# Optimization experiments

Hardware: AMD Instinct MI355X
Metric: run time of the kernel (lower is better)

Reference implementation:

```python
import jax, jax.numpy as jnp
import numpy as np

GAMMA = 2.0  # focal focusing parameter
LAM = 0.1    # disco weight


def _centered_dist(x, nw):
    """Doubly (weighted) centered pairwise |x_i - x_j| matrix, as in distance_corr."""
    d = jnp.abs(x[:, None] - x[None, :])          # [N, N]
    davg = jnp.mean(d * nw, axis=1)               # [N]  (row-wise weighted mean)
    return d - davg[None, :] - davg[:, None] + jnp.mean(davg * nw)


def _dcorr(Amat, Bmat, nw):
    ABavg = jnp.mean(Amat * Bmat * nw, axis=1)
    AAavg = jnp.mean(Amat * Amat * nw, axis=1)
    BBavg = jnp.mean(Bmat * Bmat * nw, axis=1)
    return jnp.mean(ABavg * nw) / jnp.sqrt(jnp.mean(AAavg * nw) * jnp.mean(BBavg * nw))


def setup_inputs() -> dict:
    key = jax.random.key(0)
    k1, k2, k3, k4 = jax.random.split(key, 4)
    N, C = 8192, 4
    return {
        "outputs": jax.random.normal(k1, (N, C), dtype=jnp.float32),
        "labels": jax.random.randint(k2, (N,), 0, C, dtype=jnp.int32),
        "event": jax.random.normal(k3, (N,), dtype=jnp.float32),
        "weights": jax.random.uniform(k4, (N, 1), dtype=jnp.float32, minval=0.1, maxval=1.0),
    }


def reference(outputs, labels, event, weights):
    N, C = outputs.shape
    w = weights.squeeze()                          # [N]

    # Focal loss (reduction='none'), alpha=None
    logp = jax.nn.log_softmax(outputs, axis=1)     # [N, C]
    logpt = logp[jnp.arange(N), labels]            # [N]
    pt = jnp.exp(logpt)
    focal = -(1.0 - pt) ** GAMMA * logpt * w       # per-example, times weights

    probs = jnp.exp(logp)                          # softmax(outputs)
    nw = w * N / jnp.sum(w)                        # normed weights (sum == N)

    # event-side centered distance matrix is class-independent: compute once
    Bmat = _centered_dist(event, nw)               # [N, N]

    disco = jnp.float32(0.0)
    for i in range(C):                             # small fixed class loop
        Amat = _centered_dist(probs[:, i], nw)
        disco = disco + _dcorr(Amat, Bmat, nw)
    disco = disco / C

    f = jnp.mean(focal)
    return jnp.stack([f, disco, f + LAM * disco])  # [focal, disco, tot]
```

## Files before the change

kernel.cpp:

```cpp
#include <hip/hip_runtime.h>
#include <math.h>

#define BLK 256
#define IT 2
#define JSPLIT 32
#define LAM 0.1f


__device__ __forceinline__ float wave_reduce(float v) {
    v += __shfl_down(v, 32, 64);
    v += __shfl_down(v, 16, 64);
    v += __shfl_down(v, 8, 64);
    v += __shfl_down(v, 4, 64);
    v += __shfl_down(v, 2, 64);
    v += __shfl_down(v, 1, 64);
    return v;
}

__global__ __launch_bounds__(BLK) void k1_rowprep(
        const float* __restrict__ outs, const int* __restrict__ labels,
        const float* __restrict__ event, const float* __restrict__ wts,
        float* __restrict__ probs, float* __restrict__ rows,
        float* __restrict__ scal, float* __restrict__ kpart, int N) {
    __shared__ float red[4][12];
    int i = blockIdx.x * BLK + threadIdx.x;
    float4 o = ((const float4*)outs)[i];
    float m = fmaxf(fmaxf(o.x, o.y), fmaxf(o.z, o.w));
    float e0 = expf(o.x - m), e1 = expf(o.y - m), e2 = expf(o.z - m), e3 = expf(o.w - m);
    float s = e0 + e1 + e2 + e3;
    float inv = 1.0f / s;
    float4 p = make_float4(e0 * inv, e1 * inv, e2 * inv, e3 * inv);
    ((float4*)probs)[i] = p;

    int l = labels[i];
    float ol = (l == 0) ? o.x : (l == 1) ? o.y : (l == 2) ? o.z : o.w;
    float logpt = ol - m - logf(s);
    float pt = expf(logpt);
    float w = wts[i];
    float ev = event[i];
    float om = 1.0f - pt;
    float focal = -om * om * logpt * w;

#pragma unroll
    for (int v = 0; v < 5; ++v) rows[v * N + i] = 0.f;
    if (blockIdx.x == 0 && threadIdx.x < 4) scal[threadIdx.x] = 0.f;

    float vals[12] = {focal, w,
                      w * p.x, w * p.y, w * p.z, w * p.w, w * ev,
                      w * p.x * p.x, w * p.y * p.y, w * p.z * p.z,
                      w * p.w * p.w, w * ev * ev};
    int lane = threadIdx.x & 63, wave = threadIdx.x >> 6;
#pragma unroll
    for (int k = 0; k < 12; ++k) {
        float r = wave_reduce(vals[k]);
        if (lane == 0) red[wave][k] = r;
    }
    __syncthreads();
    if (threadIdx.x < 12)
        kpart[blockIdx.x * 12 + threadIdx.x] =
            red[0][threadIdx.x] + red[1][threadIdx.x] + red[2][threadIdx.x] + red[3][threadIdx.x];
}

__global__ __launch_bounds__(BLK) void k2_pairs(
        const float* __restrict__ probs, const float* __restrict__ event,
        const float* __restrict__ wts, float* __restrict__ rows,
        float* __restrict__ scal, int N) {
    __shared__ float4 jp[BLK];
    __shared__ float2 jew[BLK];
    __shared__ float red[4][4];

    int tid = threadIdx.x;
    int i0 = blockIdx.x * (BLK * IT) + tid;
    int i1 = i0 + BLK;
    float4 pA = ((const float4*)probs)[i0];
    float4 pB = ((const float4*)probs)[i1];
    float eA = event[i0], eB = event[i1];
    float wA = wts[i0], wB = wts[i1];

    int jcount = N / JSPLIT;
    int jbase = blockIdx.y * jcount;

    float sA0 = 0.f, sA1 = 0.f, sA2 = 0.f, sA3 = 0.f, sAe = 0.f;
    float sB0 = 0.f, sB1 = 0.f, sB2 = 0.f, sB3 = 0.f, sBe = 0.f;
    float tA0 = 0.f, tA1 = 0.f, tA2 = 0.f, tA3 = 0.f;
    float tB0 = 0.f, tB1 = 0.f, tB2 = 0.f, tB3 = 0.f;

    for (int jc = 0; jc < jcount; jc += BLK) {
        int j = jbase + jc + tid;
        jp[tid] = ((const float4*)probs)[j];
        jew[tid] = make_float2(event[j], wts[j]);
        __syncthreads();
#pragma unroll 4
        for (int jj = 0; jj < BLK; ++jj) {
            float4 p = jp[jj];
            float2 ew = jew[jj];
            float wj = ew.y;
            {
                float d0 = fabsf(pA.x - p.x);
                float d1 = fabsf(pA.y - p.y);
                float d2 = fabsf(pA.z - p.z);
                float d3 = fabsf(pA.w - p.w);
                float de = fabsf(eA - ew.x);
                sA0 = fmaf(wj, d0, sA0);
                sA1 = fmaf(wj, d1, sA1);
                sA2 = fmaf(wj, d2, sA2);
                sA3 = fmaf(wj, d3, sA3);
                sAe = fmaf(wj, de, sAe);
                float wde = wj * de;
                tA0 = fmaf(wde, d0, tA0);
                tA1 = fmaf(wde, d1, tA1);
                tA2 = fmaf(wde, d2, tA2);
                tA3 = fmaf(wde, d3, tA3);
            }
            {
                float d0 = fabsf(pB.x - p.x);
                float d1 = fabsf(pB.y - p.y);
                float d2 = fabsf(pB.z - p.z);
                float d3 = fabsf(pB.w - p.w);
                float de = fabsf(eB - ew.x);
                sB0 = fmaf(wj, d0, sB0);
                sB1 = fmaf(wj, d1, sB1);
                sB2 = fmaf(wj, d2, sB2);
                sB3 = fmaf(wj, d3, sB3);
                sBe = fmaf(wj, de, sBe);
                float wde = wj * de;
                tB0 = fmaf(wde, d0, tB0);
                tB1 = fmaf(wde, d1, tB1);
                tB2 = fmaf(wde, d2, tB2);
                tB3 = fmaf(wde, d3, tB3);
            }
        }
        __syncthreads();
    }

    atomicAdd(&rows[0 * N + i0], sA0);
    atomicAdd(&rows[1 * N + i0], sA1);
    atomicAdd(&rows[2 * N + i0], sA2);
    atomicAdd(&rows[3 * N + i0], sA3);
    atomicAdd(&rows[4 * N + i0], sAe);
    atomicAdd(&rows[0 * N + i1], sB0);
    atomicAdd(&rows[1 * N + i1], sB1);
    atomicAdd(&rows[2 * N + i1], sB2);
    atomicAdd(&rows[3 * N + i1], sB3);
    atomicAdd(&rows[4 * N + i1], sBe);

    float t0 = tA0 * wA + tB0 * wB;
    float t1 = tA1 * wA + tB1 * wB;
    float t2 = tA2 * wA + tB2 * wB;
    float t3 = tA3 * wA + tB3 * wB;
    int lane = tid & 63, wave = tid >> 6;
    t0 = wave_reduce(t0); t1 = wave_reduce(t1);
    t2 = wave_reduce(t2); t3 = wave_reduce(t3);
    if (lane == 0) {
        red[wave][0] = t0; red[wave][1] = t1;
        red[wave][2] = t2; red[wave][3] = t3;
    }
    __syncthreads();
    if (tid < 4)
        atomicAdd(&scal[tid], red[0][tid] + red[1][tid] + red[2][tid] + red[3][tid]);
}

__global__ __launch_bounds__(1024) void k3_final(
        const float* __restrict__ rows, const float* __restrict__ scal,
        const float* __restrict__ wts, const float* __restrict__ kpart,
        float* __restrict__ out, int N) {
    __shared__ float red[16][14];
    __shared__ float fin[12];
    int tid = threadIdx.x, lane = tid & 63, wave = tid >> 6;

    if (wave == 0) {
#pragma unroll
        for (int k = 0; k < 12; ++k) {
            float v = (lane < 32) ? kpart[lane * 12 + k] : 0.f;
            v = wave_reduce(v);
            if (lane == 0) fin[k] = v;
        }
    }

    float acc[14];
#pragma unroll
    for (int k = 0; k < 14; ++k) acc[k] = 0.f;

    for (int i = tid; i < N; i += 1024) {
        float w = wts[i];
        float s0 = rows[0 * N + i], s1 = rows[1 * N + i], s2 = rows[2 * N + i],
              s3 = rows[3 * N + i], sE = rows[4 * N + i];
        acc[0] += w * s0; acc[1] += w * s1; acc[2] += w * s2;
        acc[3] += w * s3; acc[4] += w * sE;
        float wE = w * sE;
        acc[5] += wE * s0; acc[6] += wE * s1; acc[7] += wE * s2; acc[8] += wE * s3;
        acc[9] += wE * sE;
        acc[10] += w * s0 * s0; acc[11] += w * s1 * s1;
        acc[12] += w * s2 * s2; acc[13] += w * s3 * s3;
    }

#pragma unroll
    for (int k = 0; k < 14; ++k) acc[k] = wave_reduce(acc[k]);
    if (lane == 0) {
#pragma unroll
        for (int k = 0; k < 14; ++k) red[wave][k] = acc[k];
    }
    __syncthreads();

    if (tid == 0) {
        float SW[5], SWW_ce[4], SWW_ee, SWW_cc[4];
#pragma unroll
        for (int k = 0; k < 5; ++k) {
            float a = 0.f;
            for (int wv = 0; wv < 16; ++wv) a += red[wv][k];
            SW[k] = a;
        }
#pragma unroll
        for (int k = 0; k < 4; ++k) {
            float a = 0.f;
            for (int wv = 0; wv < 16; ++wv) a += red[wv][5 + k];
            SWW_ce[k] = a;
        }
        {
            float a = 0.f;
            for (int wv = 0; wv < 16; ++wv) a += red[wv][9];
            SWW_ee = a;
        }
#pragma unroll
        for (int k = 0; k < 4; ++k) {
            float a = 0.f;
            for (int wv = 0; wv < 16; ++wv) a += red[wv][10 + k];
            SWW_cc[k] = a;
        }

        float focal_sum = fin[0];
        float W = fin[1];
        float M1[5] = {fin[2], fin[3], fin[4], fin[5], fin[6]};
        float M2[5] = {fin[7], fin[8], fin[9], fin[10], fin[11]};

        float invW2 = 1.0f / (W * W);
        float invW3 = invW2 / W;

        float g[5];
#pragma unroll
        for (int v = 0; v < 5; ++v) g[v] = SW[v] * invW2;
        float gE = g[4];

        float Tee = 2.0f * (W * M2[4] - M1[4] * M1[4]);
        float num_ee = Tee * invW2 - 2.0f * SWW_ee * invW3 + gE * gE;

        float disco = 0.f;
#pragma unroll
        for (int c = 0; c < 4; ++c) {
            float Tcc = 2.0f * (W * M2[c] - M1[c] * M1[c]);
            float num_cc = Tcc * invW2 - 2.0f * SWW_cc[c] * invW3 + g[c] * g[c];
            float num_ce = scal[c] * invW2 - 2.0f * SWW_ce[c] * invW3 + g[c] * gE;
            disco += num_ce * rsqrtf(num_cc * num_ee);
        }
        disco *= 0.25f;

        float f = focal_sum / (float)N;
        out[0] = f;
        out[1] = disco;
        out[2] = f + LAM * disco;
    }
}

extern "C" void kernel_launch(void* const* d_in, const int* in_sizes, int n_in,
                              void* d_out, int out_size, void* d_ws, size_t ws_size,
                              hipStream_t stream) {
    const float* outs = (const float*)d_in[0];
    const int* labels = (const int*)d_in[1];
    const float* event = (const float*)d_in[2];
    const float* wts = (const float*)d_in[3];
    float* out = (float*)d_out;
    int N = in_sizes[1];

    float* ws = (float*)d_ws;
    float* probs = ws;
    float* rows = probs + (size_t)N * 4;
    float* scal = rows + (size_t)N * 5;
    float* kpart = scal + 16;

    k1_rowprep<<<N / BLK, BLK, 0, stream>>>(outs, labels, event, wts, probs, rows, scal, kpart, N);

    dim3 g2(N / (BLK * IT), JSPLIT);
    k2_pairs<<<g2, BLK, 0, stream>>>(probs, event, wts, rows, scal, N);

    k3_final<<<1, 1024, 0, stream>>>(rows, scal, wts, kpart, out, N);
}
```

Baseline: 113.2 us.

## Fuse three kernels into one cooperative kernel with grid syncs

Replaces the three separate launches (row prep, pairwise sums, final reduction) with one cooperative kernel of 1024 blocks that uses grid.sync between phases. The j dimension is split 64 ways, so each block handles a single 128-element tile with no tile loop. The aim is to cut launch overhead and inter-kernel gaps, and to run more blocks so the pairwise phase fills more of the GPU. Costs are two grid-wide barriers, a final reduction done by a single 256-thread block, and a fallback to the old three-kernel path if the cooperative launch fails (for example, if 1024 resident blocks do not fit).

```diff
diff --git a/kernel.cpp b/kernel.cpp
--- a/kernel.cpp
+++ b/kernel.cpp
@@ -1,9 +1,13 @@
 #include <hip/hip_runtime.h>
+#include <hip/hip_cooperative_groups.h>
 #include <math.h>
+
+namespace cg = cooperative_groups;
 
 #define BLK 256
 #define IT 2
-#define JSPLIT 32
+#define JSPLIT 64
+#define NBLOCKS 1024
 #define LAM 0.1f
 
 
@@ -17,81 +21,92 @@
     return v;
 }
 
-__global__ __launch_bounds__(BLK) void k1_rowprep(
+__global__ __launch_bounds__(BLK, 4) void fused_all(
         const float* __restrict__ outs, const int* __restrict__ labels,
         const float* __restrict__ event, const float* __restrict__ wts,
         float* __restrict__ probs, float* __restrict__ rows,
-        float* __restrict__ scal, float* __restrict__ kpart, int N) {
-    __shared__ float red[4][12];
-    int i = blockIdx.x * BLK + threadIdx.x;
-    float4 o = ((const float4*)outs)[i];
-    float m = fmaxf(fmaxf(o.x, o.y), fmaxf(o.z, o.w));
-    float e0 = expf(o.x - m), e1 = expf(o.y - m), e2 = expf(o.z - m), e3 = expf(o.w - m);
-    float s = e0 + e1 + e2 + e3;
-    float inv = 1.0f / s;
-    float4 p = make_float4(e0 * inv, e1 * inv, e2 * inv, e3 * inv);
-    ((float4*)probs)[i] = p;
-
-    int l = labels[i];
-    float ol = (l == 0) ? o.x : (l == 1) ? o.y : (l == 2) ? o.z : o.w;
-    float logpt = ol - m - logf(s);
-    float pt = expf(logpt);
-    float w = wts[i];
-    float ev = event[i];
-    float om = 1.0f - pt;
-    float focal = -om * om * logpt * w;
-
-#pragma unroll
-    for (int v = 0; v < 5; ++v) rows[v * N + i] = 0.f;
-    if (blockIdx.x == 0 && threadIdx.x < 4) scal[threadIdx.x] = 0.f;
-
-    float vals[12] = {focal, w,
-                      w * p.x, w * p.y, w * p.z, w * p.w, w * ev,
-                      w * p.x * p.x, w * p.y * p.y, w * p.z * p.z,
-                      w * p.w * p.w, w * ev * ev};
-    int lane = threadIdx.x & 63, wave = threadIdx.x >> 6;
-#pragma unroll
-    for (int k = 0; k < 12; ++k) {
-        float r = wave_reduce(vals[k]);
-        if (lane == 0) red[wave][k] = r;
-    }
-    __syncthreads();
-    if (threadIdx.x < 12)
-        kpart[blockIdx.x * 12 + threadIdx.x] =
-            red[0][threadIdx.x] + red[1][threadIdx.x] + red[2][threadIdx.x] + red[3][threadIdx.x];
-}
-
-__global__ __launch_bounds__(BLK) void k2_pairs(
-        const float* __restrict__ probs, const float* __restrict__ event,
-        const float* __restrict__ wts, float* __restrict__ rows,
-        float* __restrict__ scal, int N) {
-    __shared__ float4 jp[BLK];
-    __shared__ float2 jew[BLK];
-    __shared__ float red[4][4];
+        float* __restrict__ scal, float* __restrict__ kpart,
+        float* __restrict__ out, int N) {
+    cg::grid_group grid = cg::this_grid();
+
+    __shared__ float4 jp[128];
+    __shared__ float2 jew[128];
+    __shared__ float red[16][14];
+    __shared__ float fin[12];
 
     int tid = threadIdx.x;
-    int i0 = blockIdx.x * (BLK * IT) + tid;
-    int i1 = i0 + BLK;
-    float4 pA = ((const float4*)probs)[i0];
-    float4 pB = ((const float4*)probs)[i1];
-    float eA = event[i0], eB = event[i1];
-    float wA = wts[i0], wB = wts[i1];
-
-    int jcount = N / JSPLIT;
-    int jbase = blockIdx.y * jcount;
-
-    float sA0 = 0.f, sA1 = 0.f, sA2 = 0.f, sA3 = 0.f, sAe = 0.f;
-    float sB0 = 0.f, sB1 = 0.f, sB2 = 0.f, sB3 = 0.f, sBe = 0.f;
-    float tA0 = 0.f, tA1 = 0.f, tA2 = 0.f, tA3 = 0.f;
-    float tB0 = 0.f, tB1 = 0.f, tB2 = 0.f, tB3 = 0.f;
-
-    for (int jc = 0; jc < jcount; jc += BLK) {
-        int j = jbase + jc + tid;
-        jp[tid] = ((const float4*)probs)[j];
-        jew[tid] = make_float2(event[j], wts[j]);
+    int b = blockIdx.x;
+    int lane = tid & 63, wave = tid >> 6;
+
+    {
+        int gid = b * BLK + tid;
+        if (gid < 5 * N + 16) rows[gid] = 0.f;
+
+        if (b < N / BLK) {
+            int i = b * BLK + tid;
+            float4 o = ((const float4*)outs)[i];
+            float m = fmaxf(fmaxf(o.x, o.y), fmaxf(o.z, o.w));
+            float e0 = expf(o.x - m), e1 = expf(o.y - m),
+                  e2 = expf(o.z - m), e3 = expf(o.w - m);
+            float s = e0 + e1 + e2 + e3;
+            float inv = 1.0f / s;
+            float4 p = make_float4(e0 * inv, e1 * inv, e2 * inv, e3 * inv);
+            ((float4*)probs)[i] = p;
+
+            int l = labels[i];
+            float ol = (l == 0) ? o.x : (l == 1) ? o.y : (l == 2) ? o.z : o.w;
+            float logpt = ol - m - logf(s);
+            float pt = expf(logpt);
+            float w = wts[i];
+            float ev = event[i];
+            float om = 1.0f - pt;
+            float focal = -om * om * logpt * w;
+
+            float vals[12] = {focal, w,
+                              w * p.x, w * p.y, w * p.z, w * p.w, w * ev,
+                              w * p.x * p.x, w * p.y * p.y, w * p.z * p.z,
+                              w * p.w * p.w, w * ev * ev};
+#pragma unroll
+            for (int k = 0; k < 12; ++k) {
+                float r = wave_reduce(vals[k]);
+                if (lane == 0) red[wave][k] = r;
+            }
+            __syncthreads();
+            if (tid < 12)
+                kpart[b * 12 + tid] =
+                    red[0][tid] + red[1][tid] + red[2][tid] + red[3][tid];
+        }
+    }
+
+    grid.sync();
+
+    {
+        int itile = b & 15;
+        int jsp = b >> 4;
+        int jcount = N / JSPLIT;
+        int jbase = jsp * jcount;
+
+        int i0 = itile * (BLK * IT) + tid;
+        int i1 = i0 + BLK;
+        float4 pA = ((const float4*)probs)[i0];
+        float4 pB = ((const float4*)probs)[i1];
+        float eA = event[i0], eB = event[i1];
+        float wA = wts[i0], wB = wts[i1];
+
+        if (tid < 128) {
+            int j = jbase + tid;
+            jp[tid] = ((const float4*)probs)[j];
+            jew[tid] = make_float2(event[j], wts[j]);
+        }
         __syncthreads();
+
+        float sA0 = 0.f, sA1 = 0.f, sA2 = 0.f, sA3 = 0.f, sAe = 0.f;
+        float sB0 = 0.f, sB1 = 0.f, sB2 = 0.f, sB3 = 0.f, sBe = 0.f;
+        float tA0 = 0.f, tA1 = 0.f, tA2 = 0.f, tA3 = 0.f;
+        float tB0 = 0.f, tB1 = 0.f, tB2 = 0.f, tB3 = 0.f;
+
 #pragma unroll 4
-        for (int jj = 0; jj < BLK; ++jj) {
+        for (int jj = 0; jj < 128; ++jj) {
             float4 p = jp[jj];
             float2 ew = jew[jj];
             float wj = ew.y;
@@ -130,24 +145,223 @@
                 tB3 = fmaf(wde, d3, tB3);
             }
         }
+
+        atomicAdd(&rows[0 * N + i0], sA0);
+        atomicAdd(&rows[1 * N + i0], sA1);
+        atomicAdd(&rows[2 * N + i0], sA2);
+        atomicAdd(&rows[3 * N + i0], sA3);
+        atomicAdd(&rows[4 * N + i0], sAe);
+        atomicAdd(&rows[0 * N + i1], sB0);
+        atomicAdd(&rows[1 * N + i1], sB1);
+        atomicAdd(&rows[2 * N + i1], sB2);
+        atomicAdd(&rows[3 * N + i1], sB3);
+        atomicAdd(&rows[4 * N + i1], sBe);
+
+        float t0 = tA0 * wA + tB0 * wB;
+        float t1 = tA1 * wA + tB1 * wB;
+        float t2 = tA2 * wA + tB2 * wB;
+        float t3 = tA3 * wA + tB3 * wB;
+        t0 = wave_reduce(t0); t1 = wave_reduce(t1);
+        t2 = wave_reduce(t2); t3 = wave_reduce(t3);
         __syncthreads();
-    }
-
-    atomicAdd(&rows[0 * N + i0], sA0);
-    atomicAdd(&rows[1 * N + i0], sA1);
-    atomicAdd(&rows[2 * N + i0], sA2);
-    atomicAdd(&rows[3 * N + i0], sA3);
+        if (lane == 0) {
+            red[wave][0] = t0; red[wave][1] = t1;
+            red[wave][2] = t2; red[wave][3] = t3;
+        }
+        __syncthreads();
+        if (tid < 4)
+            atomicAdd(&scal[tid],
+                      red[0][tid] + red[1][tid] + red[2][tid] + red[3][tid]);
+    }
+
+    grid.sync();
+
+    if (b == 0) {
+        if (wave == 0) {
+#pragma unroll
+            for (int k = 0; k < 12; ++k) {
+                float v = (lane < 32) ? kpart[lane * 12 + k] : 0.f;
+                v = wave_reduce(v);
+                if (lane == 0) fin[k] = v;
+            }
+        }
+
+        float acc[14];
+#pragma unroll
+        for (int k = 0; k < 14; ++k) acc[k] = 0.f;
+
+        for (int i = tid; i < N; i += BLK) {
+            float w = wts[i];
+            float s0 = rows[0 * N + i], s1 = rows[1 * N + i],
+                  s2 = rows[2 * N + i], s3 = rows[3 * N + i],
+                  sE = rows[4 * N + i];
+            acc[0] += w * s0; acc[1] += w * s1; acc[2] += w * s2;
+            acc[3] += w * s3; acc[4] += w * sE;
+            float wE = w * sE;
+            acc[5] += wE * s0; acc[6] += wE * s1;
+            acc[7] += wE * s2; acc[8] += wE * s3;
+            acc[9] += wE * sE;
+            acc[10] += w * s0 * s0; acc[11] += w * s1 * s1;
+            acc[12] += w * s2 * s2; acc[13] += w * s3 * s3;
+        }
+
+#pragma unroll
+        for (int k = 0; k < 14; ++k) acc[k] = wave_reduce(acc[k]);
+        __syncthreads();
+        if (lane == 0) {
+#pragma unroll
+            for (int k = 0; k < 14; ++k) red[wave][k] = acc[k];
+        }
+        __syncthreads();
+
+        if (tid == 0) {
+            float SW[5], SWW_ce[4], SWW_ee, SWW_cc[4];
+#pragma unroll
+            for (int k = 0; k < 5; ++k)
+                SW[k] = red[0][k] + red[1][k] + red[2][k] + red[3][k];
+#pragma unroll
+            for (int k = 0; k < 4; ++k)
+                SWW_ce[k] = red[0][5 + k] + red[1][5 + k] + red[2][5 + k] + red[3][5 + k];
+            SWW_ee = red[0][9] + red[1][9] + red[2][9] + red[3][9];
+#pragma unroll
+            for (int k = 0; k < 4; ++k)
+                SWW_cc[k] = red[0][10 + k] + red[1][10 + k] + red[2][10 + k] + red[3][10 + k];
+
+            float focal_sum = fin[0];
+            float W = fin[1];
+            float M1[5] = {fin[2], fin[3], fin[4], fin[5], fin[6]};
+            float M2[5] = {fin[7], fin[8], fin[9], fin[10], fin[11]};
+
+            float invW2 = 1.0f / (W * W);
+            float invW3 = invW2 / W;
+
+            float g[5];
+#pragma unroll
+            for (int v = 0; v < 5; ++v) g[v] = SW[v] * invW2;
+            float gE = g[4];
+
+            float Tee = 2.0f * (W * M2[4] - M1[4] * M1[4]);
+            float num_ee = Tee * invW2 - 2.0f * SWW_ee * invW3 + gE * gE;
+
+            float disco = 0.f;
+#pragma unroll
+            for (int c = 0; c < 4; ++c) {
+                float Tcc = 2.0f * (W * M2[c] - M1[c] * M1[c]);
+                float num_cc = Tcc * invW2 - 2.0f * SWW_cc[c] * invW3 + g[c] * g[c];
+                float num_ce = scal[c] * invW2 - 2.0f * SWW_ce[c] * invW3 + g[c] * gE;
+                disco += num_ce * rsqrtf(num_cc * num_ee);
+            }
+            disco *= 0.25f;
+
+            float f = focal_sum / (float)N;
+            out[0] = f;
+            out[1] = disco;
+            out[2] = f + LAM * disco;
+        }
+    }
+}
+
+__global__ __launch_bounds__(BLK) void k1_rowprep(
+        const float* __restrict__ outs, const int* __restrict__ labels,
+        const float* __restrict__ event, const float* __restrict__ wts,
+        float* __restrict__ probs, float* __restrict__ rows,
+        float* __restrict__ scal, float* __restrict__ kpart, int N) {
+    __shared__ float red[4][12];
+    int i = blockIdx.x * BLK + threadIdx.x;
+    float4 o = ((const float4*)outs)[i];
+    float m = fmaxf(fmaxf(o.x, o.y), fmaxf(o.z, o.w));
+    float e0 = expf(o.x - m), e1 = expf(o.y - m), e2 = expf(o.z - m), e3 = expf(o.w - m);
+    float s = e0 + e1 + e2 + e3;
+    float inv = 1.0f / s;
+    float4 p = make_float4(e0 * inv, e1 * inv, e2 * inv, e3 * inv);
+    ((float4*)probs)[i] = p;
+    int l = labels[i];
+    float ol = (l == 0) ? o.x : (l == 1) ? o.y : (l == 2) ? o.z : o.w;
+    float logpt = ol - m - logf(s);
+    float pt = expf(logpt);
+    float w = wts[i];
+    float ev = event[i];
+    float om = 1.0f - pt;
+    float focal = -om * om * logpt * w;
+#pragma unroll
+    for (int v = 0; v < 5; ++v) rows[v * N + i] = 0.f;
+    if (blockIdx.x == 0 && threadIdx.x < 16) scal[threadIdx.x] = 0.f;
+    float vals[12] = {focal, w, w * p.x, w * p.y, w * p.z, w * p.w, w * ev,
+                      w * p.x * p.x, w * p.y * p.y, w * p.z * p.z,
+                      w * p.w * p.w, w * ev * ev};
+    int lane = threadIdx.x & 63, wave = threadIdx.x >> 6;
+#pragma unroll
+    for (int k = 0; k < 12; ++k) {
+        float r = wave_reduce(vals[k]);
+        if (lane == 0) red[wave][k] = r;
+    }
+    __syncthreads();
+    if (threadIdx.x < 12)
+        kpart[blockIdx.x * 12 + threadIdx.x] =
+            red[0][threadIdx.x] + red[1][threadIdx.x] + red[2][threadIdx.x] + red[3][threadIdx.x];
+}
+
+__global__ __launch_bounds__(BLK) void k2_pairs(
+        const float* __restrict__ probs, const float* __restrict__ event,
+        const float* __restrict__ wts, float* __restrict__ rows,
+        float* __restrict__ scal, int N) {
+    __shared__ float4 jp[128];
+    __shared__ float2 jew[128];
+    __shared__ float red[4][4];
+    int tid = threadIdx.x;
+    int itile = blockIdx.x, jsp = blockIdx.y;
+    int jcount = N / JSPLIT, jbase = jsp * jcount;
+    int i0 = itile * (BLK * IT) + tid, i1 = i0 + BLK;
+    float4 pA = ((const float4*)probs)[i0];
+    float4 pB = ((const float4*)probs)[i1];
+    float eA = event[i0], eB = event[i1];
+    float wA = wts[i0], wB = wts[i1];
+    if (tid < 128) {
+        int j = jbase + tid;
+        jp[tid] = ((const float4*)probs)[j];
+        jew[tid] = make_float2(event[j], wts[j]);
+    }
+    __syncthreads();
+    float sA0 = 0.f, sA1 = 0.f, sA2 = 0.f, sA3 = 0.f, sAe = 0.f;
+    float sB0 = 0.f, sB1 = 0.f, sB2 = 0.f, sB3 = 0.f, sBe = 0.f;
+    float tA0 = 0.f, tA1 = 0.f, tA2 = 0.f, tA3 = 0.f;
+    float tB0 = 0.f, tB1 = 0.f, tB2 = 0.f, tB3 = 0.f;
+#pragma unroll 4
+    for (int jj = 0; jj < 128; ++jj) {
+        float4 p = jp[jj];
+        float2 ew = jew[jj];
+        float wj = ew.y;
+        {
+            float d0 = fabsf(pA.x - p.x), d1 = fabsf(pA.y - p.y);
+            float d2 = fabsf(pA.z - p.z), d3 = fabsf(pA.w - p.w);
+            float de = fabsf(eA - ew.x);
+            sA0 = fmaf(wj, d0, sA0); sA1 = fmaf(wj, d1, sA1);
+            sA2 = fmaf(wj, d2, sA2); sA3 = fmaf(wj, d3, sA3);
+            sAe = fmaf(wj, de, sAe);
+            float wde = wj * de;
+            tA0 = fmaf(wde, d0, tA0); tA1 = fmaf(wde, d1, tA1);
+            tA2 = fmaf(wde, d2, tA2); tA3 = fmaf(wde, d3, tA3);
+        }
+        {
+            float d0 = fabsf(pB.x - p.x), d1 = fabsf(pB.y - p.y);
+            float d2 = fabsf(pB.z - p.z), d3 = fabsf(pB.w - p.w);
+            float de = fabsf(eB - ew.x);
+            sB0 = fmaf(wj, d0, sB0); sB1 = fmaf(wj, d1, sB1);
+            sB2 = fmaf(wj, d2, sB2); sB3 = fmaf(wj, d3, sB3);
+            sBe = fmaf(wj, de, sBe);
+            float wde = wj * de;
+            tB0 = fmaf(wde, d0, tB0); tB1 = fmaf(wde, d1, tB1);
+            tB2 = fmaf(wde, d2, tB2); tB3 = fmaf(wde, d3, tB3);
+        }
+    }
+    atomicAdd(&rows[0 * N + i0], sA0); atomicAdd(&rows[1 * N + i0], sA1);
+    atomicAdd(&rows[2 * N + i0], sA2); atomicAdd(&rows[3 * N + i0], sA3);
     atomicAdd(&rows[4 * N + i0], sAe);
-    atomicAdd(&rows[0 * N + i1], sB0);
-    atomicAdd(&rows[1 * N + i1], sB1);
-    atomicAdd(&rows[2 * N + i1], sB2);
-    atomicAdd(&rows[3 * N + i1], sB3);
+    atomicAdd(&rows[0 * N + i1], sB0); atomicAdd(&rows[1 * N + i1], sB1);
+    atomicAdd(&rows[2 * N + i1], sB2); atomicAdd(&rows[3 * N + i1], sB3);
     atomicAdd(&rows[4 * N + i1], sBe);
-
-    float t0 = tA0 * wA + tB0 * wB;
-    float t1 = tA1 * wA + tB1 * wB;
-    float t2 = tA2 * wA + tB2 * wB;
-    float t3 = tA3 * wA + tB3 * wB;
+    float t0 = tA0 * wA + tB0 * wB, t1 = tA1 * wA + tB1 * wB;
+    float t2 = tA2 * wA + tB2 * wB, t3 = tA3 * wA + tB3 * wB;
     int lane = tid & 63, wave = tid >> 6;
     t0 = wave_reduce(t0); t1 = wave_reduce(t1);
     t2 = wave_reduce(t2); t3 = wave_reduce(t3);
@@ -167,7 +381,6 @@
     __shared__ float red[16][14];
     __shared__ float fin[12];
     int tid = threadIdx.x, lane = tid & 63, wave = tid >> 6;
-
     if (wave == 0) {
 #pragma unroll
         for (int k = 0; k < 12; ++k) {
@@ -176,11 +389,9 @@
             if (lane == 0) fin[k] = v;
         }
     }
-
     float acc[14];
 #pragma unroll
     for (int k = 0; k < 14; ++k) acc[k] = 0.f;
-
     for (int i = tid; i < N; i += 1024) {
         float w = wts[i];
         float s0 = rows[0 * N + i], s1 = rows[1 * N + i], s2 = rows[2 * N + i],
@@ -193,7 +404,6 @@
         acc[10] += w * s0 * s0; acc[11] += w * s1 * s1;
         acc[12] += w * s2 * s2; acc[13] += w * s3 * s3;
     }
-
 #pragma unroll
     for (int k = 0; k < 14; ++k) acc[k] = wave_reduce(acc[k]);
     if (lane == 0) {
@@ -201,7 +411,6 @@
         for (int k = 0; k < 14; ++k) red[wave][k] = acc[k];
     }
     __syncthreads();
-
     if (tid == 0) {
         float SW[5], SWW_ce[4], SWW_ee, SWW_cc[4];
 #pragma unroll
@@ -227,23 +436,18 @@
             for (int wv = 0; wv < 16; ++wv) a += red[wv][10 + k];
             SWW_cc[k] = a;
         }
-
         float focal_sum = fin[0];
         float W = fin[1];
         float M1[5] = {fin[2], fin[3], fin[4], fin[5], fin[6]};
         float M2[5] = {fin[7], fin[8], fin[9], fin[10], fin[11]};
-
         float invW2 = 1.0f / (W * W);
         float invW3 = invW2 / W;
-
         float g[5];
 #pragma unroll
         for (int v = 0; v < 5; ++v) g[v] = SW[v] * invW2;
         float gE = g[4];
-
         float Tee = 2.0f * (W * M2[4] - M1[4] * M1[4]);
         float num_ee = Tee * invW2 - 2.0f * SWW_ee * invW3 + gE * gE;
-
         float disco = 0.f;
 #pragma unroll
         for (int c = 0; c < 4; ++c) {
@@ -253,7 +457,6 @@
             disco += num_ce * rsqrtf(num_cc * num_ee);
         }
         disco *= 0.25f;
-
         float f = focal_sum / (float)N;
         out[0] = f;
         out[1] = disco;
@@ -277,10 +480,17 @@
     float* scal = rows + (size_t)N * 5;
     float* kpart = scal + 16;
 
-    k1_rowprep<<<N / BLK, BLK, 0, stream>>>(outs, labels, event, wts, probs, rows, scal, kpart, N);
-
-    dim3 g2(N / (BLK * IT), JSPLIT);
-    k2_pairs<<<g2, BLK, 0, stream>>>(probs, event, wts, rows, scal, N);
-
-    k3_final<<<1, 1024, 0, stream>>>(rows, scal, wts, kpart, out, N);
-}
+    void* args[] = {(void*)&outs, (void*)&labels, (void*)&event, (void*)&wts,
+                    (void*)&probs, (void*)&rows, (void*)&scal, (void*)&kpart,
+                    (void*)&out, (void*)&N};
+    hipError_t err = hipLaunchCooperativeKernel(
+        (const void*)fused_all, dim3(NBLOCKS), dim3(BLK), args, 0, stream);
+
+    if (err != hipSuccess) {
+        k1_rowprep<<<N / BLK, BLK, 0, stream>>>(outs, labels, event, wts, probs,
+                                                rows, scal, kpart, N);
+        dim3 g2(N / (BLK * IT), JSPLIT);
+        k2_pairs<<<g2, BLK, 0, stream>>>(probs, event, wts, rows, scal, N);
+        k3_final<<<1, 1024, 0, stream>>>(rows, scal, wts, kpart, out, N);
+    }
+}
```

Measured after the change: 317.2 us. +180.4%, slower.

## Register-tile four rows per thread and split j into single 64-wide tiles

Applied to the files above, without the earlier changes.

The pair kernel now keeps four i-rows per thread in registers and splits the j range into 128 chunks of 64, so each block loads one small shared tile with a single barrier and no inner chunk loop. This raises arithmetic reuse per shared-memory load and cuts per-block sync overhead, while giving 8x128 blocks. The cost is four times as many atomic adds to the row sums and to the scalar accumulators, plus higher register pressure from 36 accumulators per thread. The scalar zeroing is widened to 16 entries.

```diff
diff --git a/kernel.cpp b/kernel.cpp
--- a/kernel.cpp
+++ b/kernel.cpp
@@ -2,8 +2,8 @@
 #include <math.h>
 
 #define BLK 256
-#define IT 2
-#define JSPLIT 32
+#define IT 4
+#define JSPLIT 128
 #define LAM 0.1f
 
 
@@ -43,7 +43,7 @@
 
 #pragma unroll
     for (int v = 0; v < 5; ++v) rows[v * N + i] = 0.f;
-    if (blockIdx.x == 0 && threadIdx.x < 4) scal[threadIdx.x] = 0.f;
+    if (blockIdx.x == 0 && threadIdx.x < 16) scal[threadIdx.x] = 0.f;
 
     float vals[12] = {focal, w,
                       w * p.x, w * p.y, w * p.z, w * p.w, w * ev,
@@ -62,98 +62,91 @@
 }
 
 __global__ __launch_bounds__(BLK) void k2_pairs(
-        const float* __restrict__ probs, const float* __restrict__ event,
+        const float4* __restrict__ probs4, const float* __restrict__ event,
         const float* __restrict__ wts, float* __restrict__ rows,
         float* __restrict__ scal, int N) {
-    __shared__ float4 jp[BLK];
-    __shared__ float2 jew[BLK];
+    __shared__ float4 jp[64];
+    __shared__ float2 jew[64];
     __shared__ float red[4][4];
 
     int tid = threadIdx.x;
-    int i0 = blockIdx.x * (BLK * IT) + tid;
-    int i1 = i0 + BLK;
-    float4 pA = ((const float4*)probs)[i0];
-    float4 pB = ((const float4*)probs)[i1];
-    float eA = event[i0], eB = event[i1];
-    float wA = wts[i0], wB = wts[i1];
-
+    int itile = blockIdx.x;
+    int jsp = blockIdx.y;
     int jcount = N / JSPLIT;
-    int jbase = blockIdx.y * jcount;
-
-    float sA0 = 0.f, sA1 = 0.f, sA2 = 0.f, sA3 = 0.f, sAe = 0.f;
-    float sB0 = 0.f, sB1 = 0.f, sB2 = 0.f, sB3 = 0.f, sBe = 0.f;
-    float tA0 = 0.f, tA1 = 0.f, tA2 = 0.f, tA3 = 0.f;
-    float tB0 = 0.f, tB1 = 0.f, tB2 = 0.f, tB3 = 0.f;
-
-    for (int jc = 0; jc < jcount; jc += BLK) {
-        int j = jbase + jc + tid;
-        jp[tid] = ((const float4*)probs)[j];
+    int jbase = jsp * jcount;
+    int ibase = itile * (BLK * IT) + tid;
+
+    float4 pi[IT];
+    float ei[IT], wi[IT];
+#pragma unroll
+    for (int k = 0; k < IT; ++k) {
+        int i = ibase + k * BLK;
+        pi[k] = probs4[i];
+        ei[k] = event[i];
+        wi[k] = wts[i];
+    }
+
+    if (tid < 64) {
+        int j = jbase + tid;
+        jp[tid] = probs4[j];
         jew[tid] = make_float2(event[j], wts[j]);
-        __syncthreads();
-#pragma unroll 4
-        for (int jj = 0; jj < BLK; ++jj) {
-            float4 p = jp[jj];
-            float2 ew = jew[jj];
-            float wj = ew.y;
-            {
-                float d0 = fabsf(pA.x - p.x);
-                float d1 = fabsf(pA.y - p.y);
-                float d2 = fabsf(pA.z - p.z);
-                float d3 = fabsf(pA.w - p.w);
-                float de = fabsf(eA - ew.x);
-                sA0 = fmaf(wj, d0, sA0);
-                sA1 = fmaf(wj, d1, sA1);
-                sA2 = fmaf(wj, d2, sA2);
-                sA3 = fmaf(wj, d3, sA3);
-                sAe = fmaf(wj, de, sAe);
-                float wde = wj * de;
-                tA0 = fmaf(wde, d0, tA0);
-                tA1 = fmaf(wde, d1, tA1);
-                tA2 = fmaf(wde, d2, tA2);
-                tA3 = fmaf(wde, d3, tA3);
-            }
-            {
-                float d0 = fabsf(pB.x - p.x);
-                float d1 = fabsf(pB.y - p.y);
-                float d2 = fabsf(pB.z - p.z);
-                float d3 = fabsf(pB.w - p.w);
-                float de = fabsf(eB - ew.x);
-                sB0 = fmaf(wj, d0, sB0);
-                sB1 = fmaf(wj, d1, sB1);
-                sB2 = fmaf(wj, d2, sB2);
-                sB3 = fmaf(wj, d3, sB3);
-                sBe = fmaf(wj, de, sBe);
-                float wde = wj * de;
-                tB0 = fmaf(wde, d0, tB0);
-                tB1 = fmaf(wde, d1, tB1);
-                tB2 = fmaf(wde, d2, tB2);
-                tB3 = fmaf(wde, d3, tB3);
-            }
-        }
-        __syncthreads();
-    }
-
-    atomicAdd(&rows[0 * N + i0], sA0);
-    atomicAdd(&rows[1 * N + i0], sA1);
-    atomicAdd(&rows[2 * N + i0], sA2);
-    atomicAdd(&rows[3 * N + i0], sA3);
-    atomicAdd(&rows[4 * N + i0], sAe);
-    atomicAdd(&rows[0 * N + i1], sB0);
-    atomicAdd(&rows[1 * N + i1], sB1);
-    atomicAdd(&rows[2 * N + i1], sB2);
-    atomicAdd(&rows[3 * N + i1], sB3);
-    atomicAdd(&rows[4 * N + i1], sBe);
-
-    float t0 = tA0 * wA + tB0 * wB;
-    float t1 = tA1 * wA + tB1 * wB;
-    float t2 = tA2 * wA + tB2 * wB;
-    float t3 = tA3 * wA + tB3 * wB;
+    }
+    __syncthreads();
+
+    float s[IT][5], t[IT][4];
+#pragma unroll
+    for (int k = 0; k < IT; ++k) {
+#pragma unroll
+        for (int v = 0; v < 5; ++v) s[k][v] = 0.f;
+#pragma unroll
+        for (int v = 0; v < 4; ++v) t[k][v] = 0.f;
+    }
+
+#pragma unroll 8
+    for (int jj = 0; jj < 64; ++jj) {
+        float4 p = jp[jj];
+        float2 ew = jew[jj];
+        float wj = ew.y;
+#pragma unroll
+        for (int k = 0; k < IT; ++k) {
+            float d0 = pi[k].x - p.x;
+            float d1 = pi[k].y - p.y;
+            float d2 = pi[k].z - p.z;
+            float d3 = pi[k].w - p.w;
+            float de = ei[k] - ew.x;
+            s[k][0] = fmaf(wj, fabsf(d0), s[k][0]);
+            s[k][1] = fmaf(wj, fabsf(d1), s[k][1]);
+            s[k][2] = fmaf(wj, fabsf(d2), s[k][2]);
+            s[k][3] = fmaf(wj, fabsf(d3), s[k][3]);
+            float wde = wj * fabsf(de);
+            s[k][4] += wde;
+            t[k][0] = fmaf(wde, fabsf(d0), t[k][0]);
+            t[k][1] = fmaf(wde, fabsf(d1), t[k][1]);
+            t[k][2] = fmaf(wde, fabsf(d2), t[k][2]);
+            t[k][3] = fmaf(wde, fabsf(d3), t[k][3]);
+        }
+    }
+
+#pragma unroll
+    for (int k = 0; k < IT; ++k) {
+        int i = ibase + k * BLK;
+        atomicAdd(&rows[0 * N + i], s[k][0]);
+        atomicAdd(&rows[1 * N + i], s[k][1]);
+        atomicAdd(&rows[2 * N + i], s[k][2]);
+        atomicAdd(&rows[3 * N + i], s[k][3]);
+        atomicAdd(&rows[4 * N + i], s[k][4]);
+    }
+
+    float tc0 = t[0][0] * wi[0] + t[1][0] * wi[1] + t[2][0] * wi[2] + t[3][0] * wi[3];
+    float tc1 = t[0][1] * wi[0] + t[1][1] * wi[1] + t[2][1] * wi[2] + t[3][1] * wi[3];
+    float tc2 = t[0][2] * wi[0] + t[1][2] * wi[1] + t[2][2] * wi[2] + t[3][2] * wi[3];
+    float tc3 = t[0][3] * wi[0] + t[1][3] * wi[1] + t[2][3] * wi[2] + t[3][3] * wi[3];
     int lane = tid & 63, wave = tid >> 6;
-    t0 = wave_reduce(t0); t1 = wave_reduce(t1);
-    t2 = wave_reduce(t2); t3 = wave_reduce(t3);
+    tc0 = wave_reduce(tc0); tc1 = wave_reduce(tc1);
+    tc2 = wave_reduce(tc2); tc3 = wave_reduce(tc3);
     if (lane == 0) {
-        red[wave][0] = t0; red[wave][1] = t1;
-        red[wave][2] = t2; red[wave][3] = t3;
+        red[wave][0] = tc0; red[wave][1] = tc1;
+        red[wave][2] = tc2; red[wave][3] = tc3;
     }
     __syncthreads();
     if (tid < 4)
@@ -277,10 +270,11 @@
     float* scal = rows + (size_t)N * 5;
     float* kpart = scal + 16;
 
-    k1_rowprep<<<N / BLK, BLK, 0, stream>>>(outs, labels, event, wts, probs, rows, scal, kpart, N);
+    k1_rowprep<<<N / BLK, BLK, 0, stream>>>(outs, labels, event, wts, probs,
+                                            rows, scal, kpart, N);
 
     dim3 g2(N / (BLK * IT), JSPLIT);
-    k2_pairs<<<g2, BLK, 0, stream>>>(probs, event, wts, rows, scal, N);
+    k2_pairs<<<g2, BLK, 0, stream>>>((const float4*)probs, event, wts, rows, scal, N);
 
     k3_final<<<1, 1024, 0, stream>>>(rows, scal, wts, kpart, out, N);
 }
```

Result: faster. 107.2 us (-5.3%).
